# Optimization experiments

Hardware: AMD Instinct MI355X
Metric: run time of the kernel (lower is better)

Reference implementation:

```python
import jax, jax.numpy as jnp
import numpy as np

N_HEADS = 16
HEAD_DIM = 128
ROPE_BASE = 10000.0


def _apply_rope(x, start_pos):
    # x: [B, T, H, Dh]; interleaved-pair RoPE (llama-style)
    B, T, H, Dh = x.shape
    half = Dh // 2
    inv_freq = 1.0 / (ROPE_BASE ** (jnp.arange(0, Dh, 2, dtype=jnp.float32) / Dh))  # [half]
    pos = jnp.arange(T, dtype=jnp.float32) + start_pos                              # [T]
    ang = pos[:, None] * inv_freq[None, :]                                          # [T, half]
    cos = jnp.cos(ang)[None, :, None, :].astype(x.dtype)                            # [1,T,1,half]
    sin = jnp.sin(ang)[None, :, None, :].astype(x.dtype)
    x1 = x[..., 0::2]
    x2 = x[..., 1::2]
    r1 = x1 * cos - x2 * sin
    r2 = x1 * sin + x2 * cos
    return jnp.stack([r1, r2], axis=-1).reshape(B, T, H, Dh)


def setup_inputs() -> dict:
    key = jax.random.key(0)
    k0, k1, k2, k3, k4 = jax.random.split(key, 5)
    B, T, D = 2, 2048, 2048
    d_lat = 1024
    x = jax.random.normal(k0, (B, T, D), dtype=jnp.float32)
    wq = jax.random.normal(k1, (D, N_HEADS * HEAD_DIM), dtype=jnp.float32) / np.sqrt(D)
    w_down = jax.random.normal(k2, (D, d_lat), dtype=jnp.float32) / np.sqrt(D)
    w_up = jax.random.normal(k3, (d_lat, 2 * N_HEADS * HEAD_DIM), dtype=jnp.float32) / np.sqrt(d_lat)
    wo = jax.random.normal(k4, (N_HEADS * HEAD_DIM, D), dtype=jnp.float32) / np.sqrt(N_HEADS * HEAD_DIM)
    return {"x": x, "wq": wq, "w_down": w_down, "w_up": w_up, "wo": wo}


def reference(x, wq, w_down, w_up, wo):
    # Prefill path: use_cache=False, mask=None -> causal, start_pos=0, n_kv_heads==n_heads
    B, T, D = x.shape
    H, Dh = N_HEADS, HEAD_DIM
    scale = Dh ** -0.5

    q = (x @ wq).reshape(B, T, H, Dh)
    c_kv = x @ w_down                               # [B, T, d_latent]
    kv_up = (c_kv @ w_up).reshape(B, T, H, 2 * Dh)  # latent decompression
    k, v = kv_up[..., :Dh], kv_up[..., Dh:]

    q = _apply_rope(q, 0)
    k = _apply_rope(k, 0)

    scores = jnp.einsum('bqhd,bkhd->bhqk', q, k) * scale  # [B,H,T,T]
    causal = jnp.tril(jnp.ones((T, T), dtype=bool))
    scores = jnp.where(causal[None, None, :, :], scores, jnp.float32(-jnp.inf))
    attn = jax.nn.softmax(scores, axis=-1)
    out = jnp.einsum('bhqk,bkhd->bqhd', attn, v).reshape(B, T, H * Dh)
    return out @ wo
```

## Files before the change

kernel.cpp:

```cpp
#include <hip/hip_runtime.h>
#include <math.h>
#include <stdint.h>

#define T_SEQ 2048
#define DMODEL 2048
#define DLAT 1024
#define NH 16
#define DH 128
#define BATCH 2
#define MTOT (BATCH * T_SEQ)

typedef float f32x4 __attribute__((ext_vector_type(4)));
typedef __bf16 bf16x8 __attribute__((ext_vector_type(8)));

__device__ __forceinline__ unsigned short f2bf(float f) {
    return __builtin_bit_cast(unsigned short, (__bf16)f);
}

#define EXP2F(x) __builtin_amdgcn_exp2f(x)

__device__ __forceinline__ float red16_max(float v) {
    int x = __builtin_bit_cast(int, v);
    v = fmaxf(v, __builtin_bit_cast(float, __builtin_amdgcn_update_dpp(x, x, 0xB1, 0xf, 0xf, false)));
    x = __builtin_bit_cast(int, v);
    v = fmaxf(v, __builtin_bit_cast(float, __builtin_amdgcn_update_dpp(x, x, 0x4E, 0xf, 0xf, false)));
    x = __builtin_bit_cast(int, v);
    v = fmaxf(v, __builtin_bit_cast(float, __builtin_amdgcn_update_dpp(x, x, 0x124, 0xf, 0xf, false)));
    x = __builtin_bit_cast(int, v);
    v = fmaxf(v, __builtin_bit_cast(float, __builtin_amdgcn_update_dpp(x, x, 0x128, 0xf, 0xf, false)));
    return v;
}
__device__ __forceinline__ float red16_sum(float v) {
    int x = __builtin_bit_cast(int, v);
    v += __builtin_bit_cast(float, __builtin_amdgcn_update_dpp(x, x, 0xB1, 0xf, 0xf, false));
    x = __builtin_bit_cast(int, v);
    v += __builtin_bit_cast(float, __builtin_amdgcn_update_dpp(x, x, 0x4E, 0xf, 0xf, false));
    x = __builtin_bit_cast(int, v);
    v += __builtin_bit_cast(float, __builtin_amdgcn_update_dpp(x, x, 0x124, 0xf, 0xf, false));
    x = __builtin_bit_cast(int, v);
    v += __builtin_bit_cast(float, __builtin_amdgcn_update_dpp(x, x, 0x128, 0xf, 0xf, false));
    return v;
}

#define GLL16(g, l) __builtin_amdgcn_global_load_lds( \
    (const __attribute__((address_space(1))) unsigned int*)(g), \
    (__attribute__((address_space(3))) unsigned int*)(l), 16, 0, 0)

__global__ void rope_table_kernel(float* __restrict__ cosb, float* __restrict__ sinb) {
    int idx = blockIdx.x * blockDim.x + threadIdx.x;
    if (idx >= T_SEQ * 64) return;
    int t = idx >> 6;
    int i = idx & 63;
    float inv = expf(-((2.0f * (float)i) / 128.0f) * logf(10000.0f));
    float ang = (float)t * inv;
    cosb[idx] = cosf(ang);
    sinb[idx] = sinf(ang);
}

__global__ void conv_f2b_kernel(const float* __restrict__ s, unsigned short* __restrict__ d) {
    int i = (blockIdx.x * blockDim.x + threadIdx.x) * 4;
    float4 v = *(const float4*)(s + i);
    ushort4 o;
    o.x = f2bf(v.x); o.y = f2bf(v.y); o.z = f2bf(v.z); o.w = f2bf(v.w);
    *(ushort4*)(d + i) = o;
}

__global__ __launch_bounds__(256)
void transpose_all_kernel(const float* __restrict__ wq, const float* __restrict__ wdn,
                          const float* __restrict__ wup, const float* __restrict__ wo,
                          unsigned short* __restrict__ wqT, unsigned short* __restrict__ wdT,
                          unsigned short* __restrict__ wuT, unsigned short* __restrict__ woT) {
    const int tile = blockIdx.x;
    const float* src; unsigned short* dst; int R, C, local;
    if (tile < 4096)       { src = wq;  dst = wqT; R = 2048; C = 2048; local = tile; }
    else if (tile < 6144)  { src = wdn; dst = wdT; R = 2048; C = 1024; local = tile - 4096; }
    else if (tile < 10240) { src = wup; dst = wuT; R = 1024; C = 4096; local = tile - 6144; }
    else                   { src = wo;  dst = woT; R = 2048; C = 2048; local = tile - 10240; }
    const int ctiles = C >> 5;
    const int c0 = (local & (ctiles - 1)) * 32;
    const int r0 = (local / ctiles) * 32;
    __shared__ unsigned short t16[32][33];
    const int tx = threadIdx.x & 31, ty = threadIdx.x >> 5;
#pragma unroll
    for (int i = 0; i < 32; i += 8)
        t16[ty + i][tx] = f2bf(src[(size_t)(r0 + ty + i) * C + c0 + tx]);
    __syncthreads();
#pragma unroll
    for (int i = 0; i < 32; i += 8)
        dst[(size_t)(c0 + ty + i) * R + r0 + tx] = t16[tx][ty + i];
}

__global__ void transpose_b2b_kernel(const unsigned short* __restrict__ src, unsigned short* __restrict__ dst,
                                     int R, int C) {
    __shared__ unsigned short tile[32][33];
    int tx = threadIdx.x & 31, ty = threadIdx.x >> 5;
    int r0 = blockIdx.y * 32, c0 = blockIdx.x * 32;
#pragma unroll
    for (int i = 0; i < 32; i += 8)
        tile[ty + i][tx] = src[(size_t)(r0 + ty + i) * C + c0 + tx];
    __syncthreads();
#pragma unroll
    for (int i = 0; i < 32; i += 8)
        dst[(size_t)(c0 + ty + i) * R + r0 + tx] = tile[tx][ty + i];
}

template <int EPI>
__global__ __launch_bounds__(256)
void gemm_bf16_kernel(const unsigned short* __restrict__ A, const unsigned short* __restrict__ BT,
                      void* __restrict__ C0, void* __restrict__ C1,
                      const float* __restrict__ cosb, const float* __restrict__ sinb,
                      int M, int N, int K) {
    __shared__ unsigned short As[128 * 32];
    __shared__ unsigned short Bs[128 * 32];
    const int t = threadIdx.x;
    const int w = t >> 6, l = t & 63;
    const int wr = w >> 1, wc = w & 1;
    const int lr = l & 15, lg = l >> 4;
    const int m0 = blockIdx.y * 128, n0 = blockIdx.x * 128;

    f32x4 acc[4][4] = {{}};

    const unsigned short* aP  = A  + (size_t)(m0 + (t >> 2)) * K + (t & 3) * 8;
    const unsigned short* aP2 = aP + (size_t)64 * K;
    const unsigned short* bP  = BT + (size_t)(n0 + (t >> 2)) * K + (t & 3) * 8;
    const unsigned short* bP2 = bP + (size_t)64 * K;

    for (int k0 = 0; k0 < K; k0 += 32) {
        __syncthreads();
        GLL16(aP  + k0, &As[t * 8]);
        GLL16(aP2 + k0, &As[2048 + t * 8]);
        GLL16(bP  + k0, &Bs[t * 8]);
        GLL16(bP2 + k0, &Bs[2048 + t * 8]);
        __syncthreads();

        bf16x8 af[4], bfr[4];
#pragma unroll
        for (int i = 0; i < 4; ++i)
            af[i] = *(const bf16x8*)&As[(wr * 64 + i * 16 + lr) * 32 + lg * 8];
#pragma unroll
        for (int j = 0; j < 4; ++j)
            bfr[j] = *(const bf16x8*)&Bs[(wc * 64 + j * 16 + lr) * 32 + lg * 8];
#pragma unroll
        for (int i = 0; i < 4; ++i)
#pragma unroll
            for (int j = 0; j < 4; ++j)
                acc[i][j] = __builtin_amdgcn_mfma_f32_16x16x32_bf16(af[i], bfr[j], acc[i][j], 0, 0, 0);
    }

    const float SC2 = 0.08838834764831845f * 1.44269504089f;
    const bool is_v  = (EPI == 2) && ((n0 & 128) != 0);
    const bool is_cv = (EPI == 4) && (n0 >= 2048);
#pragma unroll
    for (int i = 0; i < 4; ++i) {
#pragma unroll
        for (int j = 0; j < 4; ++j) {
#pragma unroll
            for (int rr = 0; rr < 4; ++rr) {
                const int row_g = m0 + wr * 64 + i * 16 + lg * 4 + rr;
                const int col_g = n0 + wc * 64 + j * 16 + lr;
                float v = acc[i][j][rr];
                if (EPI == 2) {
                    float res = v;
                    if (!is_v) {
                        float o_ = __shfl_xor(v, 1);
                        int d = col_g & 127;
                        int tp = row_g & (T_SEQ - 1);
                        float c = cosb[tp * 64 + (d >> 1)];
                        float s = sinb[tp * 64 + (d >> 1)];
                        res = (lr & 1) ? (o_ * s + v * c) : (v * c - o_ * s);
                    }
                    int dcol = ((col_g >> 8) << 7) | (col_g & 127);
                    unsigned short* dst = is_v ? (unsigned short*)C1 : (unsigned short*)C0;
                    dst[(size_t)row_g * DMODEL + dcol] = f2bf(res);
                } else if (EPI == 3) {
                    ((float*)C0)[(size_t)row_g * N + col_g] = v;
                } else {
                    if (!is_cv) {
                        float o_ = __shfl_xor(v, 1);
                        int d = col_g & 127;
                        int tp = row_g & (T_SEQ - 1);
                        float c = cosb[tp * 64 + (d >> 1)];
                        float s = sinb[tp * 64 + (d >> 1)];
                        float res = (lr & 1) ? (o_ * s + v * c) : (v * c - o_ * s);
                        ((unsigned short*)C0)[(size_t)row_g * DMODEL + col_g] = f2bf(res * SC2);
                    } else {
                        ((unsigned short*)C1)[(size_t)row_g * DLAT + (col_g - 2048)] = f2bf(v);
                    }
                }
            }
        }
    }
}

__global__ __launch_bounds__(256, 2)
void attn_mfma2_kernel(const unsigned short* __restrict__ qb, const unsigned short* __restrict__ kb,
                       const unsigned short* __restrict__ vT, unsigned short* __restrict__ ob) {
    __shared__ __align__(16) unsigned short Ks[64 * 128];
    __shared__ __align__(16) unsigned short Vs[128 * 64];
    __shared__ __align__(16) unsigned short Ps[4][16][64];

    const int bh = blockIdx.x;
    const int b = bh >> 4, h = bh & 15;
    const int qt = 15 - blockIdx.y;
    const int t = threadIdx.x;
    const int w = t >> 6, l = t & 63;
    const int lr = l & 15, lg = l >> 4;

    const unsigned short* kbase = kb + (size_t)(b * T_SEQ) * DMODEL + h * DH;
    const unsigned short* vbase = vT + (size_t)(h * DH) * MTOT + (size_t)b * T_SEQ;

    const int q0 = qt * 128;
    const int q_base = q0 + w * 32;

    bf16x8 qf[2][4];
#pragma unroll
    for (int rg = 0; rg < 2; ++rg) {
        const unsigned short* qrow = qb + (size_t)(b * T_SEQ + q_base + rg * 16 + lr) * DMODEL + h * DH;
#pragma unroll
        for (int c = 0; c < 4; ++c) qf[rg][c] = *(const bf16x8*)(qrow + c * 32 + lg * 8);
    }

    f32x4 o[2][8] = {{}};
    float m[2][4], lsum[2][4];
#pragma unroll
    for (int rg = 0; rg < 2; ++rg)
#pragma unroll
        for (int r = 0; r < 4; ++r) { m[rg][r] = -3.0e38f; lsum[rg][r] = 0.f; }

    const int nt = 2 * qt + 2;

    for (int kt = 0; kt < nt; ++kt) {
        const int k0 = kt * 64;
        __syncthreads();
#pragma unroll
        for (int i = 0; i < 4; ++i) {
            int c = i * 256 + t;
            int row = c >> 4;
            int k16 = (c & 15) ^ (row & 7);
            GLL16(kbase + (size_t)(k0 + row) * DMODEL + k16 * 8, &Ks[c * 8]);
        }
#pragma unroll
        for (int i = 0; i < 4; ++i) {
            int c = i * 256 + t;
            int d = c >> 3;
            int k8 = (c & 7) ^ (d & 7);
            GLL16(vbase + (size_t)d * MTOT + k0 + k8 * 8, &Vs[c * 8]);
        }
        __syncthreads();

        f32x4 s[2][4] = {{}};
        __builtin_amdgcn_s_setprio(1);
#pragma unroll
        for (int j = 0; j < 4; ++j) {
            const int krow = j * 16 + lr;
#pragma unroll
            for (int c = 0; c < 4; ++c) {
                bf16x8 kf = *(const bf16x8*)&Ks[krow * 128 + (((c * 4 + lg) ^ (krow & 7)) * 8)];
                s[0][j] = __builtin_amdgcn_mfma_f32_16x16x32_bf16(qf[0][c], kf, s[0][j], 0, 0, 0);
                s[1][j] = __builtin_amdgcn_mfma_f32_16x16x32_bf16(qf[1][c], kf, s[1][j], 0, 0, 0);
            }
        }
        __builtin_amdgcn_s_setprio(0);

#pragma unroll
        for (int rg = 0; rg < 2; ++rg) {
            const int qb0 = q_base + rg * 16;
            if (k0 + 63 > qb0) {
#pragma unroll
                for (int j = 0; j < 4; ++j) {
                    const int key = k0 + j * 16 + lr;
#pragma unroll
                    for (int r = 0; r < 4; ++r)
                        if (key > qb0 + lg * 4 + r) s[rg][j][r] = -3.0e38f;
                }
            }
            float tm[4];
            int need = 0;
#pragma unroll
            for (int r = 0; r < 4; ++r) {
                float v = fmaxf(fmaxf(s[rg][0][r], s[rg][1][r]), fmaxf(s[rg][2][r], s[rg][3][r]));
                tm[r] = red16_max(v);
                need |= (tm[r] - m[rg][r] > 8.0f) ? 1 : 0;
            }
            if (__any(need)) {
#pragma unroll
                for (int r = 0; r < 4; ++r) {
                    const float mn = fmaxf(m[rg][r], tm[r]);
                    const float a = EXP2F(m[rg][r] - mn);
                    m[rg][r] = mn;
                    lsum[rg][r] *= a;
#pragma unroll
                    for (int i = 0; i < 8; ++i) o[rg][i][r] *= a;
                }
            }
#pragma unroll
            for (int r = 0; r < 4; ++r) {
                float rs = 0.f;
#pragma unroll
                for (int j = 0; j < 4; ++j) { s[rg][j][r] = EXP2F(s[rg][j][r] - m[rg][r]); rs += s[rg][j][r]; }
                lsum[rg][r] += red16_sum(rs);
            }
        }

        bf16x8 pa[2][2];
#pragma unroll
        for (int rg = 0; rg < 2; ++rg) {
#pragma unroll
            for (int j = 0; j < 4; ++j) {
#pragma unroll
                for (int r = 0; r < 4; ++r) {
                    const int prow = lg * 4 + r;
                    const int chunk = (j * 2 + (lr >> 3)) ^ (prow & 7);
                    Ps[w][prow][chunk * 8 + (lr & 7)] = f2bf(s[rg][j][r]);
                }
            }
#pragma unroll
            for (int kc = 0; kc < 2; ++kc)
                pa[rg][kc] = *(const bf16x8*)&Ps[w][lr][((kc * 4 + lg) ^ (lr & 7)) * 8];
        }

        __builtin_amdgcn_s_setprio(1);
#pragma unroll
        for (int i = 0; i < 8; ++i) {
            const int d = i * 16 + lr;
#pragma unroll
            for (int kc = 0; kc < 2; ++kc) {
                bf16x8 vf = *(const bf16x8*)&Vs[d * 64 + (((kc * 4 + lg) ^ (d & 7)) * 8)];
                o[0][i] = __builtin_amdgcn_mfma_f32_16x16x32_bf16(pa[0][kc], vf, o[0][i], 0, 0, 0);
                o[1][i] = __builtin_amdgcn_mfma_f32_16x16x32_bf16(pa[1][kc], vf, o[1][i], 0, 0, 0);
            }
        }
        __builtin_amdgcn_s_setprio(0);
    }

#pragma unroll
    for (int rg = 0; rg < 2; ++rg) {
        float inv[4];
#pragma unroll
        for (int r = 0; r < 4; ++r) inv[r] = 1.f / lsum[rg][r];
#pragma unroll
        for (int i = 0; i < 8; ++i)
#pragma unroll
            for (int r = 0; r < 4; ++r)
                ob[(size_t)(b * T_SEQ + q_base + rg * 16 + lg * 4 + r) * DMODEL + h * DH + i * 16 + lr]
                    = f2bf(o[rg][i][r] * inv[r]);
    }
}

extern "C" void kernel_launch(void* const* d_in, const int* in_sizes, int n_in,
                              void* d_out, int out_size, void* d_ws, size_t ws_size,
                              hipStream_t stream) {
    const float* x      = (const float*)d_in[0];
    const float* wq     = (const float*)d_in[1];
    const float* w_down = (const float*)d_in[2];
    const float* w_up   = (const float*)d_in[3];
    const float* wo     = (const float*)d_in[4];
    float* out = (float*)d_out;

    uint8_t* p = (uint8_t*)d_ws;
    float* cosb = (float*)p;            p += (size_t)T_SEQ * 64 * 4;
    float* sinb = (float*)p;            p += (size_t)T_SEQ * 64 * 4;
    unsigned short* xb   = (unsigned short*)p; p += (size_t)MTOT * DMODEL * 2;
    unsigned short* wqT  = (unsigned short*)p; p += (size_t)DMODEL * DMODEL * 2;
    unsigned short* wdT  = (unsigned short*)p; p += (size_t)DLAT * DMODEL * 2;
    unsigned short* wuT  = (unsigned short*)p; p += (size_t)(2 * NH * DH) * DLAT * 2;
    unsigned short* woT  = (unsigned short*)p; p += (size_t)DMODEL * DMODEL * 2;
    unsigned short* qbuf = (unsigned short*)p; p += (size_t)MTOT * DMODEL * 2;
    unsigned short* ckv  = (unsigned short*)p; p += (size_t)MTOT * DLAT * 2;
    unsigned short* kbuf = (unsigned short*)p; p += (size_t)MTOT * DMODEL * 2;
    unsigned short* vbuf = (unsigned short*)p; p += (size_t)MTOT * DMODEL * 2;
    unsigned short* vT   = (unsigned short*)p; p += (size_t)DMODEL * MTOT * 2;
    unsigned short* abuf = xb;

    rope_table_kernel<<<(T_SEQ * 64) / 256, 256, 0, stream>>>(cosb, sinb);
    conv_f2b_kernel<<<(MTOT * DMODEL / 4) / 256, 256, 0, stream>>>(x, xb);
    transpose_all_kernel<<<14336, 256, 0, stream>>>(wq, w_down, w_up, wo, wqT, wdT, wuT, woT);

    gemm_bf16_kernel<4><<<dim3((DMODEL + DLAT) / 128, MTOT / 128), 256, 0, stream>>>(
        xb, wqT, qbuf, ckv, cosb, sinb, MTOT, DMODEL + DLAT, DMODEL);
    gemm_bf16_kernel<2><<<dim3((2 * NH * DH) / 128, MTOT / 128), 256, 0, stream>>>(
        ckv, wuT, kbuf, vbuf, cosb, sinb, MTOT, 2 * NH * DH, DLAT);
    transpose_b2b_kernel<<<dim3(DMODEL / 32, MTOT / 32), 256, 0, stream>>>(vbuf, vT, MTOT, DMODEL);
    attn_mfma2_kernel<<<dim3(BATCH * NH, 16), 256, 0, stream>>>(qbuf, kbuf, vT, abuf);
    gemm_bf16_kernel<3><<<dim3(DMODEL / 128, MTOT / 128), 256, 0, stream>>>(
        abuf, woT, out, nullptr, cosb, sinb, MTOT, DMODEL, DMODEL);
}
```

Before: 444.3 us.

## Replace GEMM with 512-thread 128x256 tile, triple-buffered async LDS pipeline

Rewrites the bf16 GEMM used for the Q/latent, up-projection and output projections. Blocks grow to 512 threads and 128x256 output tiles, with a three-stage global-to-LDS prefetch ring, vmcnt-based waits and a single barrier per k-step, an XOR swizzle on LDS chunk placement, and raised wave priority around the MFMA block. The aim is to hide global load latency behind MFMA work and reduce bank conflicts and barrier overhead. In exchange it uses more LDS per block and cuts the block count per GEMM, which could lower occupancy or leave compute units underfilled. The epilogue V/K split is re-derived from the wave column index.

```diff
diff --git a/kernel.cpp b/kernel.cpp
--- a/kernel.cpp
+++ b/kernel.cpp
@@ -105,51 +105,84 @@
 }
 
 template <int EPI>
-__global__ __launch_bounds__(256)
-void gemm_bf16_kernel(const unsigned short* __restrict__ A, const unsigned short* __restrict__ BT,
-                      void* __restrict__ C0, void* __restrict__ C1,
-                      const float* __restrict__ cosb, const float* __restrict__ sinb,
-                      int M, int N, int K) {
-    __shared__ unsigned short As[128 * 32];
-    __shared__ unsigned short Bs[128 * 32];
+__global__ __launch_bounds__(512, 2)
+void gemm8p_kernel(const unsigned short* __restrict__ A, const unsigned short* __restrict__ BT,
+                   void* __restrict__ C0, void* __restrict__ C1,
+                   const float* __restrict__ cosb, const float* __restrict__ sinb,
+                   int M, int N, int K) {
+    __shared__ __align__(16) unsigned short As3[3][128 * 32];
+    __shared__ __align__(16) unsigned short Bs3[3][256 * 32];
+
     const int t = threadIdx.x;
     const int w = t >> 6, l = t & 63;
-    const int wr = w >> 1, wc = w & 1;
+    const int wr = w >> 2, wc = w & 3;
     const int lr = l & 15, lg = l >> 4;
-    const int m0 = blockIdx.y * 128, n0 = blockIdx.x * 128;
+    const int m0 = blockIdx.y * 128, n0 = blockIdx.x * 256;
 
     f32x4 acc[4][4] = {{}};
-
-    const unsigned short* aP  = A  + (size_t)(m0 + (t >> 2)) * K + (t & 3) * 8;
-    const unsigned short* aP2 = aP + (size_t)64 * K;
-    const unsigned short* bP  = BT + (size_t)(n0 + (t >> 2)) * K + (t & 3) * 8;
-    const unsigned short* bP2 = bP + (size_t)64 * K;
-
-    for (int k0 = 0; k0 < K; k0 += 32) {
-        __syncthreads();
-        GLL16(aP  + k0, &As[t * 8]);
-        GLL16(aP2 + k0, &As[2048 + t * 8]);
-        GLL16(bP  + k0, &Bs[t * 8]);
-        GLL16(bP2 + k0, &Bs[2048 + t * 8]);
-        __syncthreads();
-
+    const int nt = K >> 5;
+
+    auto stage = [&](int kt, int buf) {
+        const int k0 = kt << 5;
+        {
+            int c = t;
+            int cc = c ^ (((c >> 5) & 1) << 1);
+            GLL16(A + (size_t)(m0 + (c >> 2)) * K + k0 + (cc & 3) * 8, &As3[buf][c * 8]);
+        }
+#pragma unroll
+        for (int u = 0; u < 2; ++u) {
+            int c = t + u * 512;
+            int cc = c ^ (((c >> 5) & 1) << 1);
+            GLL16(BT + (size_t)(n0 + (c >> 2)) * K + k0 + (cc & 3) * 8, &Bs3[buf][c * 8]);
+        }
+    };
+
+    stage(0, 0);
+    stage(1, 1);
+    asm volatile("s_waitcnt vmcnt(3)" ::: "memory");
+    __builtin_amdgcn_sched_barrier(0);
+    __builtin_amdgcn_s_barrier();
+    __builtin_amdgcn_sched_barrier(0);
+
+    int cur = 0;
+    for (int kt = 0; kt < nt; ++kt) {
+        const bool more = (kt + 2) < nt;
+        if (more) {
+            int nb = cur + 2; if (nb >= 3) nb -= 3;
+            stage(kt + 2, nb);
+        }
         bf16x8 af[4], bfr[4];
 #pragma unroll
-        for (int i = 0; i < 4; ++i)
-            af[i] = *(const bf16x8*)&As[(wr * 64 + i * 16 + lr) * 32 + lg * 8];
-#pragma unroll
-        for (int j = 0; j < 4; ++j)
-            bfr[j] = *(const bf16x8*)&Bs[(wc * 64 + j * 16 + lr) * 32 + lg * 8];
+        for (int j = 0; j < 4; ++j) {
+            int r = wc * 64 + j * 16 + lr;
+            int c = (r << 2) + lg; c ^= (((c >> 5) & 1) << 1);
+            bfr[j] = *(const bf16x8*)&Bs3[cur][c * 8];
+        }
+#pragma unroll
+        for (int i = 0; i < 4; ++i) {
+            int r = wr * 64 + i * 16 + lr;
+            int c = (r << 2) + lg; c ^= (((c >> 5) & 1) << 1);
+            af[i] = *(const bf16x8*)&As3[cur][c * 8];
+        }
+        __builtin_amdgcn_s_setprio(1);
 #pragma unroll
         for (int i = 0; i < 4; ++i)
 #pragma unroll
             for (int j = 0; j < 4; ++j)
                 acc[i][j] = __builtin_amdgcn_mfma_f32_16x16x32_bf16(af[i], bfr[j], acc[i][j], 0, 0, 0);
+        __builtin_amdgcn_s_setprio(0);
+        __builtin_amdgcn_sched_barrier(0);
+        if (more) asm volatile("s_waitcnt vmcnt(3)" ::: "memory");
+        else      asm volatile("s_waitcnt vmcnt(0)" ::: "memory");
+        __builtin_amdgcn_sched_barrier(0);
+        __builtin_amdgcn_s_barrier();
+        __builtin_amdgcn_sched_barrier(0);
+        ++cur; if (cur == 3) cur = 0;
     }
 
     const float SC2 = 0.08838834764831845f * 1.44269504089f;
-    const bool is_v  = (EPI == 2) && ((n0 & 128) != 0);
     const bool is_cv = (EPI == 4) && (n0 >= 2048);
+    const bool is_v2 = (EPI == 2) && (wc >= 2);
 #pragma unroll
     for (int i = 0; i < 4; ++i) {
 #pragma unroll
@@ -161,16 +194,16 @@
                 float v = acc[i][j][rr];
                 if (EPI == 2) {
                     float res = v;
-                    if (!is_v) {
+                    const int d = col_g & 127;
+                    if (!is_v2) {
                         float o_ = __shfl_xor(v, 1);
-                        int d = col_g & 127;
                         int tp = row_g & (T_SEQ - 1);
                         float c = cosb[tp * 64 + (d >> 1)];
                         float s = sinb[tp * 64 + (d >> 1)];
                         res = (lr & 1) ? (o_ * s + v * c) : (v * c - o_ * s);
                     }
-                    int dcol = ((col_g >> 8) << 7) | (col_g & 127);
-                    unsigned short* dst = is_v ? (unsigned short*)C1 : (unsigned short*)C0;
+                    const int dcol = ((col_g >> 8) << 7) | d;
+                    unsigned short* dst = is_v2 ? (unsigned short*)C1 : (unsigned short*)C0;
                     dst[(size_t)row_g * DMODEL + dcol] = f2bf(res);
                 } else if (EPI == 3) {
                     ((float*)C0)[(size_t)row_g * N + col_g] = v;
@@ -376,12 +409,12 @@
     conv_f2b_kernel<<<(MTOT * DMODEL / 4) / 256, 256, 0, stream>>>(x, xb);
     transpose_all_kernel<<<14336, 256, 0, stream>>>(wq, w_down, w_up, wo, wqT, wdT, wuT, woT);
 
-    gemm_bf16_kernel<4><<<dim3((DMODEL + DLAT) / 128, MTOT / 128), 256, 0, stream>>>(
+    gemm8p_kernel<4><<<dim3((DMODEL + DLAT) / 256, MTOT / 128), 512, 0, stream>>>(
         xb, wqT, qbuf, ckv, cosb, sinb, MTOT, DMODEL + DLAT, DMODEL);
-    gemm_bf16_kernel<2><<<dim3((2 * NH * DH) / 128, MTOT / 128), 256, 0, stream>>>(
+    gemm8p_kernel<2><<<dim3((2 * NH * DH) / 256, MTOT / 128), 512, 0, stream>>>(
         ckv, wuT, kbuf, vbuf, cosb, sinb, MTOT, 2 * NH * DH, DLAT);
     transpose_b2b_kernel<<<dim3(DMODEL / 32, MTOT / 32), 256, 0, stream>>>(vbuf, vT, MTOT, DMODEL);
     attn_mfma2_kernel<<<dim3(BATCH * NH, 16), 256, 0, stream>>>(qbuf, kbuf, vT, abuf);
-    gemm_bf16_kernel<3><<<dim3(DMODEL / 128, MTOT / 128), 256, 0, stream>>>(
+    gemm8p_kernel<3><<<dim3(DMODEL / 256, MTOT / 128), 512, 0, stream>>>(
         abuf, woT, out, nullptr, cosb, sinb, MTOT, DMODEL, DMODEL);
 }
```

Result: faster. 425.7 us (-4.2%).
